# Kernel tuning notes

Measured on AMD Instinct MI355X. Metric: run time of the kernel, lower is better.

## Reference

```python
import jax, jax.numpy as jnp
import numpy as np

H = 8          # head_num
NEG = -1e9     # mask fill value
LN_EPS = 1e-6


def setup_inputs() -> dict:
    key = jax.random.key(0)
    ks = jax.random.split(key, 12)
    B, S, D = 8, 1024, 512
    inp = {
        'q': jax.random.normal(ks[0], (B, S, D), jnp.float32),
        'k': jax.random.normal(ks[1], (B, S, D), jnp.float32),
        'v': jax.random.normal(ks[2], (B, S, D), jnp.float32),
        'query_mask': jax.random.randint(ks[3], (B, S), 0, 2, jnp.int32),
        'key_mask': jax.random.randint(ks[4], (B, S), 0, 2, jnp.int32),
        'Wq': jax.random.normal(ks[5], (D, D), jnp.float32) / np.sqrt(D),
        'bq': jax.random.normal(ks[6], (D,), jnp.float32) * 0.02,
        'Wk': jax.random.normal(ks[7], (D, D), jnp.float32) / np.sqrt(D),
        'bk': jax.random.normal(ks[8], (D,), jnp.float32) * 0.02,
        'Wv': jax.random.normal(ks[9], (D, D), jnp.float32) / np.sqrt(D),
        'bv': jax.random.normal(ks[10], (D,), jnp.float32) * 0.02,
        'gamma': jnp.ones((D,), jnp.float32),
        'beta': jnp.zeros((D,), jnp.float32),
    }
    return inp


def _to_batches(x):
    # [B,S,D] -> [B*H, S, D/H]  (batch-major head layout, as in torch code)
    B, S, D = x.shape
    return x.reshape(B, S, H, D // H).transpose(0, 2, 1, 3).reshape(B * H, S, D // H)


def _from_batches(x):
    BH, S, d = x.shape
    B = BH // H
    return x.reshape(B, H, S, d).transpose(0, 2, 1, 3).reshape(B, S, H * d)


def reference(q, k, v, query_mask, key_mask, Wq, bq, Wk, bk, Wv, bv, gamma, beta):
    # QKV linears + ReLU activation (activation=F.relu in original)
    _q = jax.nn.relu(q @ Wq.T + bq)
    _k = jax.nn.relu(k @ Wk.T + bk)
    _v = jax.nn.relu(v @ Wv.T + bv)
    _q, _k, _v = _to_batches(_q), _to_batches(_k), _to_batches(_v)  # [B*H,S,d]

    # masks tiled head-MAJOR (repeat(head_num,1) semantics): index = h*B + b
    km = jnp.tile(key_mask, (H, 1))[:, None, :]    # [B*H, 1, S_k]
    qm = jnp.tile(query_mask, (H, 1))[:, :, None]  # [B*H, S_q, 1]

    d = _q.shape[-1]
    scores = jnp.einsum('bqd,bkd->bqk', _q, _k) / jnp.sqrt(jnp.float32(d))
    scores = jnp.where(km == 0, NEG, scores)
    attn = jax.nn.softmax(scores, axis=-1)
    attn = attn * qm.astype(attn.dtype)            # multiplicative query mask
    # dropout: eval mode (rate applied only in training) -> identity
    y = jnp.einsum('bqk,bkd->bqd', attn, _v)
    y = _from_batches(y) + q                       # residual
    # LayerNorm over last dim
    mu = jnp.mean(y, axis=-1, keepdims=True)
    var = jnp.mean((y - mu) ** 2, axis=-1, keepdims=True)
    return gamma * (y - mu) / jnp.sqrt(var + LN_EPS) + beta
```

## Files before the change

### kernel.cpp

```cpp
#include <hip/hip_runtime.h>
#include <hip/hip_bf16.h>
#include <stdint.h>

constexpr int kB = 8, kH = 8, kS = 1024, kD = 512, kDH = 64;
constexpr float kNeg = -1e9f;
constexpr float kScaleLog2e = 0.125f * 1.4426950408889634f;

typedef __attribute__((ext_vector_type(8))) short bf16x8;
typedef __attribute__((ext_vector_type(4))) float f32x4;
typedef __attribute__((ext_vector_type(4))) unsigned short u16x4;

__device__ __forceinline__ unsigned short f2bf(float f) {
  union { float f; unsigned int u; } a; a.f = f;
  return (unsigned short)((a.u + 0x7FFFu + ((a.u >> 16) & 1u)) >> 16);
}

__device__ __forceinline__ unsigned int pk2bf(float lo, float hi) {
  union { __hip_bfloat162 h; unsigned int u; } cv;
  cv.h = __float22bfloat162_rn(make_float2(lo, hi));
  return cv.u;
}

#if __has_builtin(__builtin_amdgcn_exp2f)
#define EXP2F(x) __builtin_amdgcn_exp2f(x)
#else
#define EXP2F(x) exp2f(x)
#endif

__global__ __launch_bounds__(256)
void wcvt_kernel(const float* __restrict__ wq, const float* __restrict__ wk,
                 const float* __restrict__ wv, unsigned short* __restrict__ wout)
{
  const int tid = blockIdx.x * 256 + threadIdx.x;
  const int z = tid >> 16;
  const int i = (tid & 65535) * 4;
  const float* W = (z == 0) ? wq : (z == 1) ? wk : wv;
  float4 v4 = *(const float4*)(W + i);
  u16x4 pk;
  pk[0] = f2bf(v4.x); pk[1] = f2bf(v4.y); pk[2] = f2bf(v4.z); pk[3] = f2bf(v4.w);
  *(u16x4*)(wout + (size_t)z * 262144 + i) = pk;
}

__global__ __launch_bounds__(512)
void qkv_gemm_kernel(const float* __restrict__ xq, const float* __restrict__ xk,
                     const float* __restrict__ xv,
                     const unsigned short* __restrict__ wbf,
                     const float* __restrict__ bq, const float* __restrict__ bk,
                     const float* __restrict__ bv,
                     unsigned short* __restrict__ wsout)
{
  __shared__ __align__(16) unsigned short As[128][72];
  __shared__ __align__(16) unsigned short Bs[128][72];

  const int bid = blockIdx.x;
  const int xcd = bid & 7;
  const int j = bid >> 3;
  const int x = j & 3;
  const int g = (j >> 2) * 8 + xcd;
  const int z = g >> 6;
  const int y = g & 63;

  const float* X    = (z == 0) ? xq : (z == 1) ? xk : xv;
  const unsigned short* Wb = wbf + (size_t)z * 262144;
  const float* bias = (z == 0) ? bq : (z == 1) ? bk : bv;
  unsigned short* out = wsout + (size_t)z * (kB * kS * kD);

  const int m0 = y * 128;
  const int n0 = x * 128;
  const int t = threadIdx.x;
  const int lane = t & 63;
  const int w = t >> 6;
  const int wr = w >> 2, wc = w & 3;
  const int l16 = lane & 15, lg = lane >> 4;

  const int row = t >> 3, c8 = (t & 7) * 8;
  const int rowB = row + 64;
  const float* Xr0 = X + (size_t)(m0 + row) * kD + c8;
  const float* Xr1 = X + (size_t)(m0 + rowB) * kD + c8;
  const unsigned short* Wr0 = Wb + (size_t)(n0 + row) * kD + c8;
  const unsigned short* Wr1 = Wb + (size_t)(n0 + rowB) * kD + c8;

  f32x4 acc[4][2] = {};
  float4 pa00, pa01, pa10, pa11;
  uint4  pb00, pb01;
  float4 qa00, qa01, qa10, qa11;
  uint4  qb00, qb01;

  auto load0 = [&](int kt) {
    pa00 = *(const float4*)(Xr0 + kt);
    pa01 = *(const float4*)(Xr0 + kt + 4);
    pa10 = *(const float4*)(Xr1 + kt);
    pa11 = *(const float4*)(Xr1 + kt + 4);
    pb00 = *(const uint4*)(Wr0 + kt);
    pb01 = *(const uint4*)(Wr1 + kt);
  };
  auto load1 = [&](int kt) {
    qa00 = *(const float4*)(Xr0 + kt);
    qa01 = *(const float4*)(Xr0 + kt + 4);
    qa10 = *(const float4*)(Xr1 + kt);
    qa11 = *(const float4*)(Xr1 + kt + 4);
    qb00 = *(const uint4*)(Wr0 + kt);
    qb01 = *(const uint4*)(Wr1 + kt);
  };
  auto lds_write0 = [&]() {
    uint4 ua;
    ua.x = pk2bf(pa00.x, pa00.y); ua.y = pk2bf(pa00.z, pa00.w);
    ua.z = pk2bf(pa01.x, pa01.y); ua.w = pk2bf(pa01.z, pa01.w);
    *(uint4*)&As[row][c8] = ua;
    ua.x = pk2bf(pa10.x, pa10.y); ua.y = pk2bf(pa10.z, pa10.w);
    ua.z = pk2bf(pa11.x, pa11.y); ua.w = pk2bf(pa11.z, pa11.w);
    *(uint4*)&As[rowB][c8] = ua;
    *(uint4*)&Bs[row][c8]  = pb00;
    *(uint4*)&Bs[rowB][c8] = pb01;
  };
  auto lds_write1 = [&]() {
    uint4 ua;
    ua.x = pk2bf(qa00.x, qa00.y); ua.y = pk2bf(qa00.z, qa00.w);
    ua.z = pk2bf(qa01.x, qa01.y); ua.w = pk2bf(qa01.z, qa01.w);
    *(uint4*)&As[row][c8] = ua;
    ua.x = pk2bf(qa10.x, qa10.y); ua.y = pk2bf(qa10.z, qa10.w);
    ua.z = pk2bf(qa11.x, qa11.y); ua.w = pk2bf(qa11.z, qa11.w);
    *(uint4*)&As[rowB][c8] = ua;
    *(uint4*)&Bs[row][c8]  = qb00;
    *(uint4*)&Bs[rowB][c8] = qb01;
  };
  auto mfma_phase = [&]() {
#pragma unroll
    for (int kk = 0; kk < 2; ++kk) {
      bf16x8 av[4];
#pragma unroll
      for (int mf = 0; mf < 4; ++mf)
        av[mf] = *(const bf16x8*)&As[wr * 64 + mf * 16 + l16][kk * 32 + lg * 8];
#pragma unroll
      for (int nf = 0; nf < 2; ++nf) {
        bf16x8 bfr = *(const bf16x8*)&Bs[wc * 32 + nf * 16 + l16][kk * 32 + lg * 8];
#pragma unroll
        for (int mf = 0; mf < 4; ++mf)
          acc[mf][nf] = __builtin_amdgcn_mfma_f32_16x16x32_bf16(bfr, av[mf], acc[mf][nf], 0, 0, 0);
      }
    }
  };

  load0(0);
#pragma unroll
  for (int kt = 0; kt < 512; kt += 128) {
    __syncthreads();
    lds_write0();
    if (kt + 64 < 512) load1(kt + 64);
    __syncthreads();
    mfma_phase();
    __syncthreads();
    lds_write1();
    if (kt + 128 < 512) load0(kt + 128);
    __syncthreads();
    mfma_phase();
  }

  if (z == 2) {
    const int mmbase = m0 + wr * 64;
    const int b_ = mmbase >> 10, sbase = mmbase & 1023;
#pragma unroll
    for (int nf = 0; nf < 2; ++nf) {
#pragma unroll
      for (int r = 0; r < 4; ++r) {
        const int n = n0 + wc * 32 + nf * 16 + lg * 4 + r;
        const float bval = bias[n];
        const int h = n >> 6, dd = n & 63;
        u16x4 pk;
#pragma unroll
        for (int mf = 0; mf < 4; ++mf) {
          float vv = acc[mf][nf][r] + bval;
          vv = vv > 0.f ? vv : 0.f;
          pk[mf] = f2bf(vv);
        }
        *(u16x4*)&out[((size_t)((b_ * kH + h) * kDH + dd)) * kS + sbase + l16 * 4] = pk;
      }
    }
  } else {
#pragma unroll
    for (int mf = 0; mf < 4; ++mf) {
      const int mm = m0 + wr * 64 + mf * 16 + l16;
      const int b_ = mm >> 10, s = mm & 1023;
#pragma unroll
      for (int nf = 0; nf < 2; ++nf) {
        const int nbase = n0 + wc * 32 + nf * 16 + lg * 4;
        const int h = nbase >> 6, dd = nbase & 63;
        u16x4 pk;
#pragma unroll
        for (int r = 0; r < 4; ++r) {
          float vv = acc[mf][nf][r] + bias[nbase + r];
          vv = vv > 0.f ? vv : 0.f;
          pk[r] = f2bf(vv);
        }
        *(u16x4*)&out[((size_t)(b_ * kH + h) * kS + s) * kDH + dd] = pk;
      }
    }
  }
}

__global__ __launch_bounds__(256)
void attn_kernel(const unsigned short* __restrict__ ws,
                 const int* __restrict__ key_mask,
                 float* __restrict__ y)
{
  __shared__ __align__(16) unsigned short Ks[64][72];
  __shared__ __align__(16) unsigned short Vts[64][72];
  __shared__ __align__(16) unsigned short Ps[4][16][72];
  __shared__ float kmadd[64];

  const unsigned short* Qw = ws;
  const unsigned short* Kw = ws + (size_t)1 * kB * kS * kD;
  const unsigned short* Vw = ws + (size_t)2 * kB * kS * kD;

  const int bid = blockIdx.x;
  const int xcd = bid & 7;
  const int j = bid >> 3;
  const int qx = j & 15;
  const int bh = (j >> 4) * 8 + xcd;

  const int q0 = qx * 64;
  const int t = threadIdx.x;
  const int w = t >> 6, lane = t & 63;
  const int l16 = lane & 15, lg = lane >> 4;
  const int b_ = bh / kH, h = bh % kH;

  const unsigned short* Qb = Qw + ((size_t)bh * kS + q0) * kDH;
  const unsigned short* Kb = Kw + (size_t)bh * kS * kDH;
  const unsigned short* Vb = Vw + (size_t)bh * kDH * kS;
  const int* km = key_mask + (bh % kB) * kS;

  bf16x8 aq[2];
#pragma unroll
  for (int kk = 0; kk < 2; ++kk)
    aq[kk] = *(const bf16x8*)(Qb + (size_t)(w * 16 + l16) * kDH + kk * 32 + lg * 8);

  bf16x8 vone;
#pragma unroll
  for (int jj = 0; jj < 8; ++jj) vone[jj] = (short)0x3F80;

  f32x4 o[4] = {};
  f32x4 lacc = {};

  for (int kv0 = 0; kv0 < kS; kv0 += 64) {
    __syncthreads();
#pragma unroll
    for (int i = 0; i < 2; ++i) {
      const int c = t + 256 * i;
      const int row = c >> 3, c8 = (c & 7) * 8;
      *(uint4*)&Ks[row][c8]  = *(const uint4*)(Kb + (size_t)(kv0 + row) * kDH + c8);
      *(uint4*)&Vts[row][c8] = *(const uint4*)(Vb + (size_t)row * kS + kv0 + c8);
    }
    if (t < 64) kmadd[t] = km[kv0 + t] ? 0.f : kNeg;
    __syncthreads();

    f32x4 sc[4] = {};
#pragma unroll
    for (int kk = 0; kk < 2; ++kk) {
#pragma unroll
      for (int nf = 0; nf < 4; ++nf) {
        bf16x8 bfr = *(const bf16x8*)&Ks[nf * 16 + l16][kk * 32 + lg * 8];
        sc[nf] = __builtin_amdgcn_mfma_f32_16x16x32_bf16(aq[kk], bfr, sc[nf], 0, 0, 0);
      }
    }

    float madd[4];
#pragma unroll
    for (int nf = 0; nf < 4; ++nf) madd[nf] = kmadd[nf * 16 + l16];

#pragma unroll
    for (int r = 0; r < 4; ++r) {
      const float p0 = EXP2F(fmaf(sc[0][r], kScaleLog2e, madd[0]));
      const float p1 = EXP2F(fmaf(sc[1][r], kScaleLog2e, madd[1]));
      const float p2 = EXP2F(fmaf(sc[2][r], kScaleLog2e, madd[2]));
      const float p3 = EXP2F(fmaf(sc[3][r], kScaleLog2e, madd[3]));
      const int prow = lg * 4 + r;
      uint2 pw;
      pw.x = __builtin_amdgcn_perm(__float_as_uint(p1), __float_as_uint(p0), 0x07060302u);
      pw.y = __builtin_amdgcn_perm(__float_as_uint(p3), __float_as_uint(p2), 0x07060302u);
      *(uint2*)&Ps[w][prow][l16 * 4] = pw;
    }

#pragma unroll
    for (int kk = 0; kk < 2; ++kk) {
      bf16x8 a = *(const bf16x8*)&Ps[w][l16][kk * 32 + lg * 8];
#pragma unroll
      for (int nd = 0; nd < 4; ++nd) {
        bf16x8 bfr = *(const bf16x8*)&Vts[nd * 16 + l16][kk * 32 + lg * 8];
        o[nd] = __builtin_amdgcn_mfma_f32_16x16x32_bf16(a, bfr, o[nd], 0, 0, 0);
      }
      lacc = __builtin_amdgcn_mfma_f32_16x16x32_bf16(a, vone, lacc, 0, 0, 0);
    }
  }

  float rinv[4];
#pragma unroll
  for (int r = 0; r < 4; ++r) rinv[r] = 1.f / lacc[r];
#pragma unroll
  for (int nd = 0; nd < 4; ++nd) {
#pragma unroll
    for (int r = 0; r < 4; ++r) {
      const int srow = q0 + w * 16 + lg * 4 + r;
      y[((size_t)b_ * kS + srow) * kD + h * kDH + nd * 16 + l16] = o[nd][r] * rinv[r];
    }
  }
}

__global__ __launch_bounds__(256)
void ln_kernel(const float* __restrict__ y, const float* __restrict__ q,
               const int* __restrict__ qmask,
               const float* __restrict__ gamma, const float* __restrict__ beta,
               float* __restrict__ out)
{
  const int w = threadIdx.x >> 6, lane = threadIdx.x & 63;
  const int row = blockIdx.x * 4 + w;
  const int b_ = row >> 10, s = row & 1023;
  const int d0 = lane * 8;
  const int h = d0 >> 6;

  const float* yp = y + (size_t)row * kD + d0;
  const float* qp = q + (size_t)row * kD + d0;
  const int qm = qmask[((b_ * kH + h) % kB) * kS + s];

  float4 y0 = *(const float4*)yp, y1 = *(const float4*)(yp + 4);
  float4 q0 = *(const float4*)qp, q1 = *(const float4*)(qp + 4);
  float vals[8] = { y0.x, y0.y, y0.z, y0.w, y1.x, y1.y, y1.z, y1.w };
  float qs[8]   = { q0.x, q0.y, q0.z, q0.w, q1.x, q1.y, q1.z, q1.w };

  float sum = 0.f, ss = 0.f;
#pragma unroll
  for (int j = 0; j < 8; ++j) {
    const float val = (qm ? vals[j] : 0.f) + qs[j];
    vals[j] = val; sum += val; ss += val * val;
  }
#pragma unroll
  for (int off = 1; off < 64; off <<= 1) {
    sum += __shfl_xor(sum, off);
    ss  += __shfl_xor(ss, off);
  }
  const float mu = sum * (1.f / kD);
  const float var = ss * (1.f / kD) - mu * mu;
  const float rstd = rsqrtf(var + 1e-6f);

  float4 g0 = *(const float4*)(gamma + d0), g1 = *(const float4*)(gamma + d0 + 4);
  float4 be0 = *(const float4*)(beta + d0), be1 = *(const float4*)(beta + d0 + 4);
  float gs[8] = { g0.x, g0.y, g0.z, g0.w, g1.x, g1.y, g1.z, g1.w };
  float bs[8] = { be0.x, be0.y, be0.z, be0.w, be1.x, be1.y, be1.z, be1.w };

  float4 o0, o1;
  o0.x = gs[0] * (vals[0] - mu) * rstd + bs[0];
  o0.y = gs[1] * (vals[1] - mu) * rstd + bs[1];
  o0.z = gs[2] * (vals[2] - mu) * rstd + bs[2];
  o0.w = gs[3] * (vals[3] - mu) * rstd + bs[3];
  o1.x = gs[4] * (vals[4] - mu) * rstd + bs[4];
  o1.y = gs[5] * (vals[5] - mu) * rstd + bs[5];
  o1.z = gs[6] * (vals[6] - mu) * rstd + bs[6];
  o1.w = gs[7] * (vals[7] - mu) * rstd + bs[7];
  *(float4*)(out + (size_t)row * kD + d0) = o0;
  *(float4*)(out + (size_t)row * kD + d0 + 4) = o1;
}

extern "C" void kernel_launch(void* const* d_in, const int* in_sizes, int n_in,
                              void* d_out, int out_size, void* d_ws, size_t ws_size,
                              hipStream_t stream) {
  const float* q  = (const float*)d_in[0];
  const float* k  = (const float*)d_in[1];
  const float* v  = (const float*)d_in[2];
  const int* qmask = (const int*)d_in[3];
  const int* kmask = (const int*)d_in[4];
  const float* Wq = (const float*)d_in[5];
  const float* bq = (const float*)d_in[6];
  const float* Wk = (const float*)d_in[7];
  const float* bk = (const float*)d_in[8];
  const float* Wv = (const float*)d_in[9];
  const float* bv = (const float*)d_in[10];
  const float* gamma = (const float*)d_in[11];
  const float* beta  = (const float*)d_in[12];
  float* out = (float*)d_out;
  unsigned short* wsqkv = (unsigned short*)d_ws;
  unsigned short* wbf = (unsigned short*)d_out;

  wcvt_kernel<<<768, 256, 0, stream>>>(Wq, Wk, Wv, wbf);
  qkv_gemm_kernel<<<768, 512, 0, stream>>>(
      q, k, v, wbf, bq, bk, bv, wsqkv);
  attn_kernel<<<1024, 256, 0, stream>>>(wsqkv, kmask, out);
  ln_kernel<<<2048, 256, 0, stream>>>(out, q, qmask, gamma, beta, out);
}
```

Baseline: 77.62 us.

## Register-prefetch next K/V tile in attention loop to overlap loads with compute

The attention kernel now loads the next 64-key K/V tile and key-mask values into registers before computing the current tile, using two register sets that alternate across an unrolled-by-two loop. The global load latency can then overlap with the MFMA and exp work. Compiler memory fences are added after the load groups in both the projection GEMM and attention loaders so the loads are issued early and not sunk toward their uses. In exchange the kernel uses more registers, which may lower occupancy.

```diff
diff --git a/kernel.cpp b/kernel.cpp
--- a/kernel.cpp
+++ b/kernel.cpp
@@ -20,6 +20,8 @@
   cv.h = __float22bfloat162_rn(make_float2(lo, hi));
   return cv.u;
 }
+
+__device__ __forceinline__ void memfence_compiler() { asm volatile("" ::: "memory"); }
 
 #if __has_builtin(__builtin_amdgcn_exp2f)
 #define EXP2F(x) __builtin_amdgcn_exp2f(x)
@@ -93,6 +95,7 @@
     pa11 = *(const float4*)(Xr1 + kt + 4);
     pb00 = *(const uint4*)(Wr0 + kt);
     pb01 = *(const uint4*)(Wr1 + kt);
+    memfence_compiler();
   };
   auto load1 = [&](int kt) {
     qa00 = *(const float4*)(Xr0 + kt);
@@ -101,6 +104,7 @@
     qa11 = *(const float4*)(Xr1 + kt + 4);
     qb00 = *(const uint4*)(Wr0 + kt);
     qb01 = *(const uint4*)(Wr1 + kt);
+    memfence_compiler();
   };
   auto lds_write0 = [&]() {
     uint4 ua;
@@ -229,6 +233,12 @@
   const unsigned short* Vb = Vw + (size_t)bh * kDH * kS;
   const int* km = key_mask + (bh % kB) * kS;
 
+  const int srow = t >> 3, sc8 = (t & 7) * 8;
+  const unsigned short* KbR0 = Kb + (size_t)srow * kDH + sc8;
+  const unsigned short* KbR1 = Kb + (size_t)(srow + 32) * kDH + sc8;
+  const unsigned short* VbR0 = Vb + (size_t)srow * kS + sc8;
+  const unsigned short* VbR1 = Vb + (size_t)(srow + 32) * kS + sc8;
+
   bf16x8 aq[2];
 #pragma unroll
   for (int kk = 0; kk < 2; ++kk)
@@ -241,18 +251,40 @@
   f32x4 o[4] = {};
   f32x4 lacc = {};
 
-  for (int kv0 = 0; kv0 < kS; kv0 += 64) {
-    __syncthreads();
-#pragma unroll
-    for (int i = 0; i < 2; ++i) {
-      const int c = t + 256 * i;
-      const int row = c >> 3, c8 = (c & 7) * 8;
-      *(uint4*)&Ks[row][c8]  = *(const uint4*)(Kb + (size_t)(kv0 + row) * kDH + c8);
-      *(uint4*)&Vts[row][c8] = *(const uint4*)(Vb + (size_t)row * kS + kv0 + c8);
-    }
-    if (t < 64) kmadd[t] = km[kv0 + t] ? 0.f : kNeg;
-    __syncthreads();
-
+  uint4 ka0, ka1, va0, va1; int kma;
+  uint4 kb0, kb1, vb0, vb1; int kmb;
+
+  auto loadA = [&](int kv0) {
+    ka0 = *(const uint4*)(KbR0 + (size_t)kv0 * kDH);
+    ka1 = *(const uint4*)(KbR1 + (size_t)kv0 * kDH);
+    va0 = *(const uint4*)(VbR0 + kv0);
+    va1 = *(const uint4*)(VbR1 + kv0);
+    kma = (t < 64) ? km[kv0 + t] : 0;
+    memfence_compiler();
+  };
+  auto loadB = [&](int kv0) {
+    kb0 = *(const uint4*)(KbR0 + (size_t)kv0 * kDH);
+    kb1 = *(const uint4*)(KbR1 + (size_t)kv0 * kDH);
+    vb0 = *(const uint4*)(VbR0 + kv0);
+    vb1 = *(const uint4*)(VbR1 + kv0);
+    kmb = (t < 64) ? km[kv0 + t] : 0;
+    memfence_compiler();
+  };
+  auto writeA = [&]() {
+    *(uint4*)&Ks[srow][sc8]       = ka0;
+    *(uint4*)&Ks[srow + 32][sc8]  = ka1;
+    *(uint4*)&Vts[srow][sc8]      = va0;
+    *(uint4*)&Vts[srow + 32][sc8] = va1;
+    if (t < 64) kmadd[t] = kma ? 0.f : kNeg;
+  };
+  auto writeB = [&]() {
+    *(uint4*)&Ks[srow][sc8]       = kb0;
+    *(uint4*)&Ks[srow + 32][sc8]  = kb1;
+    *(uint4*)&Vts[srow][sc8]      = vb0;
+    *(uint4*)&Vts[srow + 32][sc8] = vb1;
+    if (t < 64) kmadd[t] = kmb ? 0.f : kNeg;
+  };
+  auto compute = [&]() {
     f32x4 sc[4] = {};
 #pragma unroll
     for (int kk = 0; kk < 2; ++kk) {
@@ -262,11 +294,9 @@
         sc[nf] = __builtin_amdgcn_mfma_f32_16x16x32_bf16(aq[kk], bfr, sc[nf], 0, 0, 0);
       }
     }
-
     float madd[4];
 #pragma unroll
     for (int nf = 0; nf < 4; ++nf) madd[nf] = kmadd[nf * 16 + l16];
-
 #pragma unroll
     for (int r = 0; r < 4; ++r) {
       const float p0 = EXP2F(fmaf(sc[0][r], kScaleLog2e, madd[0]));
@@ -279,7 +309,6 @@
       pw.y = __builtin_amdgcn_perm(__float_as_uint(p3), __float_as_uint(p2), 0x07060302u);
       *(uint2*)&Ps[w][prow][l16 * 4] = pw;
     }
-
 #pragma unroll
     for (int kk = 0; kk < 2; ++kk) {
       bf16x8 a = *(const bf16x8*)&Ps[w][l16][kk * 32 + lg * 8];
@@ -290,6 +319,20 @@
       }
       lacc = __builtin_amdgcn_mfma_f32_16x16x32_bf16(a, vone, lacc, 0, 0, 0);
     }
+  };
+
+  loadA(0);
+  for (int kv0 = 0; kv0 < kS; kv0 += 128) {
+    __syncthreads();
+    writeA();
+    if (kv0 + 64 < kS) loadB(kv0 + 64);
+    __syncthreads();
+    compute();
+    __syncthreads();
+    writeB();
+    if (kv0 + 128 < kS) loadA(kv0 + 128);
+    __syncthreads();
+    compute();
   }
 
   float rinv[4];
@@ -299,8 +342,8 @@
   for (int nd = 0; nd < 4; ++nd) {
 #pragma unroll
     for (int r = 0; r < 4; ++r) {
-      const int srow = q0 + w * 16 + lg * 4 + r;
-      y[((size_t)b_ * kS + srow) * kD + h * kDH + nd * 16 + l16] = o[nd][r] * rinv[r];
+      const int srowq = q0 + w * 16 + lg * 4 + r;
+      y[((size_t)b_ * kS + srowq) * kD + h * kDH + nd * 16 + l16] = o[nd][r] * rinv[r];
     }
   }
 }
```

Result: no change. 77.82 us (+0.3%).
